# Performance work log

Measured on AMD Instinct MI355X. Metric: run time of the kernel, lower is better.

Reference implementation:

```python
import jax, jax.numpy as jnp
import numpy as np

D = 128       # in_features
H = 256       # hidden
OUT = 128     # out_features
NUM_STEPS = 3
K = 8         # k_neighbors (k = min(K, N))


def setup_inputs() -> dict:
    key = jax.random.key(0)
    ks = jax.random.split(key, 12)
    s = 0.02
    return {
        "x":    jax.random.normal(ks[0], (4, 4096, D), dtype=jnp.float32),
        # neighbor_proj: Linear(D -> H)
        "Wn":   jax.random.normal(ks[1], (D, H), dtype=jnp.float32) * s,
        "bn":   jnp.zeros((H,), dtype=jnp.float32),
        # local_rule[0]: Linear(D + H -> H)
        "W1":   jax.random.normal(ks[2], (D + H, H), dtype=jnp.float32) * s,
        "b1":   jnp.zeros((H,), dtype=jnp.float32),
        # local_rule[1]: LayerNorm(H)
        "ln_g": jnp.ones((H,), dtype=jnp.float32),
        "ln_b": jnp.zeros((H,), dtype=jnp.float32),
        # local_rule[3]: Linear(H -> D)
        "W2":   jax.random.normal(ks[3], (H, D), dtype=jnp.float32) * s,
        "b2":   jnp.zeros((D,), dtype=jnp.float32),
        # out_proj: Linear(D -> OUT)
        "Wo":   jax.random.normal(ks[4], (D, OUT), dtype=jnp.float32) * s,
        "bo":   jnp.zeros((OUT,), dtype=jnp.float32),
    }


def _layernorm(h, g, b, eps=1e-5):
    mu = jnp.mean(h, axis=-1, keepdims=True)
    var = jnp.var(h, axis=-1, keepdims=True)
    return (h - mu) * jax.lax.rsqrt(var + eps) * g + b


def reference(x, Wn, bn, W1, b1, ln_g, ln_b, W2, b2, Wo, bo):
    B, N, _ = x.shape
    k = min(K, N)
    batch_ix = jnp.arange(B)[:, None, None]  # (B,1,1)
    state = x
    for _ in range(NUM_STEPS):
        keys = state @ Wn + bn                                     # (B,N,H)
        keys = keys / jnp.maximum(
            jnp.linalg.norm(keys, axis=-1, keepdims=True), 1e-12)  # F.normalize
        sim = jnp.einsum('bnh,bmh->bnm', keys, keys)               # (B,N,N)
        _, idx = jax.lax.top_k(sim, k)                             # (B,N,k)
        gathered = state[batch_ix, idx]                            # (B,N,k,D)
        neighbor_agg = gathered.mean(axis=2) @ Wn + bn             # (B,N,H)
        combined = jnp.concatenate([state, neighbor_agg], axis=-1) # (B,N,D+H)
        h = _layernorm(combined @ W1 + b1, ln_g, ln_b)
        update = jax.nn.silu(h) @ W2 + b2                          # (B,N,D)
        state = state + update
    return state.mean(axis=1) @ Wo + bo                            # (B,OUT)
```

## Files before the change

### kernel.cpp

```cpp
#include <hip/hip_runtime.h>

#define DDIM 128
#define HDIM 256
#define BQ   4
#define NN   4096
#define RTOT (BQ*NN)

typedef short short8 __attribute__((ext_vector_type(8)));
typedef short short4v __attribute__((ext_vector_type(4)));
typedef float f32x16 __attribute__((ext_vector_type(16)));

__device__ inline unsigned short f2bf(float f) {
    unsigned int u = __float_as_uint(f);
    unsigned int r = (u + 0x7fffu + ((u >> 16) & 1u)) >> 16;
    return (unsigned short)r;
}
__device__ inline float bf2f(unsigned short h) {
    return __uint_as_float(((unsigned int)h) << 16);
}

#define MFMA32(a, b, c) __builtin_amdgcn_mfma_f32_32x32x16_bf16(a, b, c, 0, 0, 0)

__global__ void pack_w_kernel(const float* __restrict__ W, int N,
                              unsigned short* __restrict__ ph, unsigned short* __restrict__ pl) {
    int l = threadIdx.x, l31 = l & 31, lh = l >> 5;
    int nt = N >> 5;
    int t = blockIdx.x / nt, c = blockIdx.x % nt;
    short8 hv, lv;
#pragma unroll
    for (int j = 0; j < 8; ++j) {
        float f = W[(size_t)(t * 16 + lh * 8 + j) * N + c * 32 + l31];
        unsigned short h = f2bf(f);
        hv[j] = (short)h;
        lv[j] = (short)f2bf(f - bf2f(h));
    }
    *(short8*)(ph + (size_t)(blockIdx.x * 64 + l) * 8) = hv;
    *(short8*)(pl + (size_t)(blockIdx.x * 64 + l) * 8) = lv;
}

__global__ __launch_bounds__(256, 2)
void sim_topk_kernel(const unsigned short* __restrict__ khi,
                     const unsigned short* __restrict__ klo,
                     int* __restrict__ idxout) {
    __shared__ __align__(16) char smem[4 * 4 * 4096];

    const int id = blockIdx.x;
    const int xcd = id & 7;
    const int b = xcd >> 1;
    const int j = ((id >> 3) << 1) | (xcd & 1);
    const int rowbase = j * 32;
    const unsigned short* khiB = khi + (size_t)b * NN * HDIM;
    const unsigned short* kloB = klo + (size_t)b * NN * HDIM;

    const int tid = threadIdx.x;
    const int lane = tid & 63, w = tid >> 6;
    const int l31 = lane & 31, lh = lane >> 5;

    short8 ah[16], al[16];
    {
        const unsigned short* ph = khiB + (size_t)(rowbase + l31) * HDIM + lh * 8;
        const unsigned short* pl = kloB + (size_t)(rowbase + l31) * HDIM + lh * 8;
#pragma unroll
        for (int T = 0; T < 16; ++T) {
            ah[T] = *(const short8*)(ph + T * 16);
            al[T] = *(const short8*)(pl + T * 16);
        }
    }
#pragma unroll
    for (int T = 0; T < 16; ++T) {
        asm volatile("" : "+v"(ah[T]));
        asm volatile("" : "+v"(al[T]));
    }

    char* mybuf = smem + w * 16384;

    const int sc8 = lane >> 3, sg8 = lane & 7;
    auto stage = [&](int s) {
        const int cs2 = s >> 3, sub = s & 7;
        const int kb2 = sub >> 1;
        const unsigned short* pb = (sub & 1) ? kloB : khiB;
        char* dst = mybuf + (s & 3) * 4096;
        const int c0 = w * 1024 + cs2 * 32;
#pragma unroll
        for (int i = 0; i < 4; ++i) {
            const unsigned short* src =
                pb + (size_t)(c0 + i * 8 + sc8) * HDIM + kb2 * 64 + ((sg8 ^ sc8) * 8);
            __builtin_amdgcn_global_load_lds(
                (const __attribute__((address_space(1))) void*)src,
                (__attribute__((address_space(3))) void*)(dst + i * 1024), 16, 0, 0);
        }
    };

    stage(0);
    stage(1);
    stage(2);

    const int key = l31 & 7;
    const int rbase = l31 * 128;
    const int sl0 = (((0) * 2 + lh) ^ key) * 16;
    const int sl1 = (((1) * 2 + lh) ^ key) * 16;
    const int sl2 = (((2) * 2 + lh) ^ key) * 16;
    const int sl3 = (((3) * 2 + lh) ^ key) * 16;

    float tv[8]; int ti[8];
#pragma unroll
    for (int s = 0; s < 8; ++s) { tv[s] = -1e30f; ti[s] = 0x7fffffff; }

    for (int cs = 0; cs < 32; ++cs) {
        f32x16 acc;
#pragma unroll
        for (int r = 0; r < 16; ++r) acc[r] = 0.f;

#pragma unroll
        for (int sub = 0; sub < 8; ++sub) {
            const int s = cs * 8 + sub;
            if (s < 254)       asm volatile("s_waitcnt vmcnt(8)" ::: "memory");
            else if (s == 254) asm volatile("s_waitcnt vmcnt(4)" ::: "memory");
            else               asm volatile("s_waitcnt vmcnt(0)" ::: "memory");

            const char* bufc = mybuf + (s & 3) * 4096;
            short8 B0 = *(const short8*)(bufc + rbase + sl0);
            short8 B1 = *(const short8*)(bufc + rbase + sl1);
            short8 B2 = *(const short8*)(bufc + rbase + sl2);
            short8 B3 = *(const short8*)(bufc + rbase + sl3);
            asm volatile("s_waitcnt lgkmcnt(4)" ::: "memory");
            if (s + 3 < 256) stage(s + 3);

            const int T0 = (sub >> 1) * 4;
            if ((sub & 1) == 0) {
                acc = MFMA32(B0, ah[T0],     acc);
                acc = MFMA32(B0, al[T0],     acc);
                acc = MFMA32(B1, ah[T0 + 1], acc);
                acc = MFMA32(B1, al[T0 + 1], acc);
                acc = MFMA32(B2, ah[T0 + 2], acc);
                acc = MFMA32(B2, al[T0 + 2], acc);
                acc = MFMA32(B3, ah[T0 + 3], acc);
                acc = MFMA32(B3, al[T0 + 3], acc);
            } else {
                acc = MFMA32(B0, ah[T0],     acc);
                acc = MFMA32(B1, ah[T0 + 1], acc);
                acc = MFMA32(B2, ah[T0 + 2], acc);
                acc = MFMA32(B3, ah[T0 + 3], acc);
            }
        }

        const int cbase = w * 1024 + cs * 32 + 4 * lh;
#pragma unroll
        for (int r = 0; r < 16; ++r) {
            float v = acc[r];
            int col = cbase + (r & 3) + 8 * (r >> 2);
            if (v > tv[7]) {
                tv[7] = v; ti[7] = col;
#pragma unroll
                for (int q = 7; q >= 1; --q) {
                    if (tv[q] > tv[q - 1]) {
                        float a0 = tv[q]; tv[q] = tv[q - 1]; tv[q - 1] = a0;
                        int   c0_ = ti[q]; ti[q] = ti[q - 1]; ti[q - 1] = c0_;
                    }
                }
            }
        }
    }

    __syncthreads();
    float* vbuf = (float*)smem;
    int*   ibuf = (int*)(smem + 32 * 66 * 4);
    const int list = w * 2 + lh;
#pragma unroll
    for (int s = 0; s < 8; ++s) {
        vbuf[l31 * 66 + list * 8 + s] = tv[s];
        ibuf[l31 * 66 + list * 8 + s] = ti[s];
    }
    __syncthreads();
    if (tid < 32) {
        float fv[8]; int fi[8];
#pragma unroll
        for (int s = 0; s < 8; ++s) { fv[s] = -1e30f; fi[s] = 0x7fffffff; }
        for (int e = 0; e < 64; ++e) {
            float v = vbuf[tid * 66 + e];
            int  ix = ibuf[tid * 66 + e];
            bool ins = (v > fv[7]) || (v == fv[7] && ix < fi[7]);
            if (ins) {
                fv[7] = v; fi[7] = ix;
#pragma unroll
                for (int q = 7; q >= 1; --q) {
                    bool sw = (fv[q] > fv[q - 1]) || (fv[q] == fv[q - 1] && fi[q] < fi[q - 1]);
                    if (sw) {
                        float a0 = fv[q]; fv[q] = fv[q - 1]; fv[q - 1] = a0;
                        int   c0_ = fi[q]; fi[q] = fi[q - 1]; fi[q - 1] = c0_;
                    }
                }
            }
        }
        size_t basei = ((size_t)b * NN + rowbase + tid) * 8;
#pragma unroll
        for (int s = 0; s < 8; ++s) idxout[basei + s] = fi[s];
    }
}

__global__ __launch_bounds__(256, 2)
void gemm_keys_mfma(const float* __restrict__ A,
                    const unsigned short* __restrict__ wh, const unsigned short* __restrict__ wl,
                    const float* __restrict__ bias,
                    unsigned short* __restrict__ khi, unsigned short* __restrict__ klo) {
    __shared__ float ssqbuf[2][32][2];
    const int tid = threadIdx.x, lane = tid & 63, w = tid >> 6;
    const int l31 = lane & 31, lh = lane >> 5;
    const int rw = w & 1, cw = w >> 1;
    const int row = blockIdx.x * 64 + rw * 32 + l31;

    short8 ahi[8], alo[8];
    const float* ap = A + (size_t)row * DDIM + lh * 8;
#pragma unroll
    for (int T = 0; T < 8; ++T) {
        float4 f0 = *(const float4*)(ap + T * 16);
        float4 f1 = *(const float4*)(ap + T * 16 + 4);
        float ff[8] = {f0.x, f0.y, f0.z, f0.w, f1.x, f1.y, f1.z, f1.w};
#pragma unroll
        for (int j2 = 0; j2 < 8; ++j2) {
            unsigned short h = f2bf(ff[j2]);
            ahi[T][j2] = (short)h;
            alo[T][j2] = (short)f2bf(ff[j2] - bf2f(h));
        }
    }

    f32x16 acc[4];
#pragma unroll
    for (int ct = 0; ct < 4; ++ct)
#pragma unroll
        for (int r = 0; r < 16; ++r) acc[ct][r] = 0.f;

#pragma unroll
    for (int T = 0; T < 8; ++T) {
#pragma unroll
        for (int ct = 0; ct < 4; ++ct) {
            const size_t pi = (size_t)((T * 8 + cw * 4 + ct) * 64 + lane) * 8;
            short8 bh = *(const short8*)(wh + pi);
            short8 bl = *(const short8*)(wl + pi);
            acc[ct] = MFMA32(bh, ahi[T], acc[ct]);
            acc[ct] = MFMA32(bl, ahi[T], acc[ct]);
            acc[ct] = MFMA32(bh, alo[T], acc[ct]);
        }
    }

    float ss = 0.f;
#pragma unroll
    for (int ct = 0; ct < 4; ++ct)
#pragma unroll
        for (int g = 0; g < 4; ++g) {
            const int c0 = cw * 128 + ct * 32 + g * 8 + lh * 4;
            float4 bz = *(const float4*)(bias + c0);
            float bzf[4] = {bz.x, bz.y, bz.z, bz.w};
#pragma unroll
            for (int j2 = 0; j2 < 4; ++j2) {
                acc[ct][g * 4 + j2] += bzf[j2];
                ss += acc[ct][g * 4 + j2] * acc[ct][g * 4 + j2];
            }
        }
    ss += __shfl_xor(ss, 32);
    if (lh == 0) ssqbuf[rw][l31][cw] = ss;
    __syncthreads();
    float sstot = ssqbuf[rw][l31][0] + ssqbuf[rw][l31][1];
    float scn = 1.0f / fmaxf(sqrtf(sstot), 1e-12f);

#pragma unroll
    for (int ct = 0; ct < 4; ++ct)
#pragma unroll
        for (int g = 0; g < 4; ++g) {
            const int c0 = cw * 128 + ct * 32 + g * 8 + lh * 4;
            short4v hv, lv;
#pragma unroll
            for (int j2 = 0; j2 < 4; ++j2) {
                float vn = acc[ct][g * 4 + j2] * scn;
                unsigned short h = f2bf(vn);
                hv[j2] = (short)h;
                lv[j2] = (short)f2bf(vn - bf2f(h));
            }
            *(short4v*)(khi + (size_t)row * HDIM + c0) = hv;
            *(short4v*)(klo + (size_t)row * HDIM + c0) = lv;
        }
}

__global__ __launch_bounds__(256, 2)
void gemm_agg_mfma(const float* __restrict__ state, const int* __restrict__ idx,
                   const unsigned short* __restrict__ wh, const unsigned short* __restrict__ wl,
                   const float* __restrict__ bias,
                   unsigned short* __restrict__ oh, unsigned short* __restrict__ ol) {
    const int tid = threadIdx.x, lane = tid & 63, w = tid >> 6;
    const int l31 = lane & 31, lh = lane >> 5;
    const int rw = w & 1, cw = w >> 1;
    const int row = blockIdx.x * 64 + rw * 32 + l31;
    const int bb = row >> 12;
    const float* sb = state + (size_t)bb * NN * DDIM;
    const int* mi = idx + (size_t)row * 8;

    int ridx[8];
#pragma unroll
    for (int k = 0; k < 8; ++k) ridx[k] = mi[k];

    short8 ahi[8], alo[8];
#pragma unroll
    for (int T = 0; T < 8; ++T) {
        float fr[8] = {0.f, 0.f, 0.f, 0.f, 0.f, 0.f, 0.f, 0.f};
#pragma unroll
        for (int k = 0; k < 8; ++k) {
            const float* rp = sb + (size_t)ridx[k] * DDIM + T * 16 + lh * 8;
            float4 f0 = *(const float4*)rp;
            float4 f1 = *(const float4*)(rp + 4);
            fr[0] += f0.x; fr[1] += f0.y; fr[2] += f0.z; fr[3] += f0.w;
            fr[4] += f1.x; fr[5] += f1.y; fr[6] += f1.z; fr[7] += f1.w;
        }
#pragma unroll
        for (int j2 = 0; j2 < 8; ++j2) {
            float v = fr[j2] * 0.125f;
            unsigned short h = f2bf(v);
            ahi[T][j2] = (short)h;
            alo[T][j2] = (short)f2bf(v - bf2f(h));
        }
    }

    f32x16 acc[4];
#pragma unroll
    for (int ct = 0; ct < 4; ++ct)
#pragma unroll
        for (int r = 0; r < 16; ++r) acc[ct][r] = 0.f;

#pragma unroll
    for (int T = 0; T < 8; ++T) {
#pragma unroll
        for (int ct = 0; ct < 4; ++ct) {
            const size_t pi = (size_t)((T * 8 + cw * 4 + ct) * 64 + lane) * 8;
            short8 bh = *(const short8*)(wh + pi);
            short8 bl = *(const short8*)(wl + pi);
            acc[ct] = MFMA32(bh, ahi[T], acc[ct]);
            acc[ct] = MFMA32(bl, ahi[T], acc[ct]);
            acc[ct] = MFMA32(bh, alo[T], acc[ct]);
        }
    }

#pragma unroll
    for (int ct = 0; ct < 4; ++ct)
#pragma unroll
        for (int g = 0; g < 4; ++g) {
            const int c0 = cw * 128 + ct * 32 + g * 8 + lh * 4;
            float4 bz = *(const float4*)(bias + c0);
            float bzf[4] = {bz.x, bz.y, bz.z, bz.w};
            short4v hv, lv;
#pragma unroll
            for (int j2 = 0; j2 < 4; ++j2) {
                float vn = acc[ct][g * 4 + j2] + bzf[j2];
                unsigned short h = f2bf(vn);
                hv[j2] = (short)h;
                lv[j2] = (short)f2bf(vn - bf2f(h));
            }
            *(short4v*)(oh + (size_t)row * HDIM + c0) = hv;
            *(short4v*)(ol + (size_t)row * HDIM + c0) = lv;
        }
}

__global__ __launch_bounds__(256, 2)
void gemm_ln_mfma(const float* __restrict__ state,
                  const unsigned short* __restrict__ agh, const unsigned short* __restrict__ agl,
                  const unsigned short* __restrict__ wh, const unsigned short* __restrict__ wl,
                  const float* __restrict__ b1, const float* __restrict__ lng,
                  const float* __restrict__ lnb,
                  unsigned short* __restrict__ gh, unsigned short* __restrict__ gl) {
    __shared__ float s1buf[2][32][2], s2buf[2][32][2];
    const int tid = threadIdx.x, lane = tid & 63, w = tid >> 6;
    const int l31 = lane & 31, lh = lane >> 5;
    const int rw = w & 1, cw = w >> 1;
    const int row = blockIdx.x * 64 + rw * 32 + l31;

    f32x16 acc[4];
#pragma unroll
    for (int ct = 0; ct < 4; ++ct)
#pragma unroll
        for (int r = 0; r < 16; ++r) acc[ct][r] = 0.f;

    short8 ahi[8], alo[8];
    {
        const float* ap = state + (size_t)row * DDIM + lh * 8;
#pragma unroll
        for (int T = 0; T < 8; ++T) {
            float4 f0 = *(const float4*)(ap + T * 16);
            float4 f1 = *(const float4*)(ap + T * 16 + 4);
            float ff[8] = {f0.x, f0.y, f0.z, f0.w, f1.x, f1.y, f1.z, f1.w};
#pragma unroll
            for (int j2 = 0; j2 < 8; ++j2) {
                unsigned short h = f2bf(ff[j2]);
                ahi[T][j2] = (short)h;
                alo[T][j2] = (short)f2bf(ff[j2] - bf2f(h));
            }
        }
#pragma unroll
        for (int T = 0; T < 8; ++T)
#pragma unroll
            for (int ct = 0; ct < 4; ++ct) {
                const size_t pi = (size_t)((T * 8 + cw * 4 + ct) * 64 + lane) * 8;
                short8 bh = *(const short8*)(wh + pi);
                short8 bl = *(const short8*)(wl + pi);
                acc[ct] = MFMA32(bh, ahi[T], acc[ct]);
                acc[ct] = MFMA32(bl, ahi[T], acc[ct]);
                acc[ct] = MFMA32(bh, alo[T], acc[ct]);
            }
    }
#pragma unroll
    for (int kc = 1; kc < 3; ++kc) {
#pragma unroll
        for (int T = 0; T < 8; ++T) {
            ahi[T] = *(const short8*)(agh + (size_t)row * HDIM + (kc - 1) * 128 + T * 16 + lh * 8);
            alo[T] = *(const short8*)(agl + (size_t)row * HDIM + (kc - 1) * 128 + T * 16 + lh * 8);
        }
#pragma unroll
        for (int T = 0; T < 8; ++T)
#pragma unroll
            for (int ct = 0; ct < 4; ++ct) {
                const size_t pi = (size_t)(((kc * 8 + T) * 8 + cw * 4 + ct) * 64 + lane) * 8;
                short8 bh = *(const short8*)(wh + pi);
                short8 bl = *(const short8*)(wl + pi);
                acc[ct] = MFMA32(bh, ahi[T], acc[ct]);
                acc[ct] = MFMA32(bl, ahi[T], acc[ct]);
                acc[ct] = MFMA32(bh, alo[T], acc[ct]);
            }
    }

    float s1 = 0.f, s2 = 0.f;
#pragma unroll
    for (int ct = 0; ct < 4; ++ct)
#pragma unroll
        for (int g = 0; g < 4; ++g) {
            const int c0 = cw * 128 + ct * 32 + g * 8 + lh * 4;
            float4 bz = *(const float4*)(b1 + c0);
            float bzf[4] = {bz.x, bz.y, bz.z, bz.w};
#pragma unroll
            for (int j2 = 0; j2 < 4; ++j2) {
                acc[ct][g * 4 + j2] += bzf[j2];
                s1 += acc[ct][g * 4 + j2];
                s2 += acc[ct][g * 4 + j2] * acc[ct][g * 4 + j2];
            }
        }
    s1 += __shfl_xor(s1, 32);
    s2 += __shfl_xor(s2, 32);
    if (lh == 0) { s1buf[rw][l31][cw] = s1; s2buf[rw][l31][cw] = s2; }
    __syncthreads();
    float s1t = s1buf[rw][l31][0] + s1buf[rw][l31][1];
    float s2t = s2buf[rw][l31][0] + s2buf[rw][l31][1];
    float mu = s1t * (1.0f / HDIM);
    float var = s2t * (1.0f / HDIM) - mu * mu;
    float inv = 1.0f / sqrtf(var + 1e-5f);

#pragma unroll
    for (int ct = 0; ct < 4; ++ct)
#pragma unroll
        for (int g = 0; g < 4; ++g) {
            const int c0 = cw * 128 + ct * 32 + g * 8 + lh * 4;
            float4 gg = *(const float4*)(lng + c0);
            float4 bb = *(const float4*)(lnb + c0);
            float ggf[4] = {gg.x, gg.y, gg.z, gg.w};
            float bbf[4] = {bb.x, bb.y, bb.z, bb.w};
            short4v hv, lv;
#pragma unroll
            for (int j2 = 0; j2 < 4; ++j2) {
                float hval = (acc[ct][g * 4 + j2] - mu) * inv * ggf[j2] + bbf[j2];
                float gval = hval / (1.0f + expf(-hval));
                unsigned short h = f2bf(gval);
                hv[j2] = (short)h;
                lv[j2] = (short)f2bf(gval - bf2f(h));
            }
            *(short4v*)(gh + (size_t)row * HDIM + c0) = hv;
            *(short4v*)(gl + (size_t)row * HDIM + c0) = lv;
        }
}

__global__ __launch_bounds__(256, 2)
void gemm_upd_mfma(const unsigned short* __restrict__ gh, const unsigned short* __restrict__ gl,
                   const unsigned short* __restrict__ wh, const unsigned short* __restrict__ wl,
                   const float* __restrict__ b2, float* __restrict__ state) {
    const int tid = threadIdx.x, lane = tid & 63, w = tid >> 6;
    const int l31 = lane & 31, lh = lane >> 5;
    const int rw = w & 1, cw = w >> 1;
    const int row = blockIdx.x * 64 + rw * 32 + l31;

    f32x16 acc[2];
#pragma unroll
    for (int ct = 0; ct < 2; ++ct)
#pragma unroll
        for (int r = 0; r < 16; ++r) acc[ct][r] = 0.f;

    short8 ahi[8], alo[8];
#pragma unroll
    for (int kc = 0; kc < 2; ++kc) {
#pragma unroll
        for (int T = 0; T < 8; ++T) {
            ahi[T] = *(const short8*)(gh + (size_t)row * HDIM + kc * 128 + T * 16 + lh * 8);
            alo[T] = *(const short8*)(gl + (size_t)row * HDIM + kc * 128 + T * 16 + lh * 8);
        }
#pragma unroll
        for (int T = 0; T < 8; ++T)
#pragma unroll
            for (int ct = 0; ct < 2; ++ct) {
                const size_t pi = (size_t)(((kc * 8 + T) * 4 + cw * 2 + ct) * 64 + lane) * 8;
                short8 bh = *(const short8*)(wh + pi);
                short8 bl = *(const short8*)(wl + pi);
                acc[ct] = MFMA32(bh, ahi[T], acc[ct]);
                acc[ct] = MFMA32(bl, ahi[T], acc[ct]);
                acc[ct] = MFMA32(bh, alo[T], acc[ct]);
            }
    }

#pragma unroll
    for (int ct = 0; ct < 2; ++ct)
#pragma unroll
        for (int g = 0; g < 4; ++g) {
            const int c0 = cw * 64 + ct * 32 + g * 8 + lh * 4;
            float4 bz = *(const float4*)(b2 + c0);
            float bzf[4] = {bz.x, bz.y, bz.z, bz.w};
            float4* sp = (float4*)(state + (size_t)row * DDIM + c0);
            float4 sv = *sp;
            float svf[4] = {sv.x, sv.y, sv.z, sv.w};
#pragma unroll
            for (int j2 = 0; j2 < 4; ++j2) svf[j2] += acc[ct][g * 4 + j2] + bzf[j2];
            sv.x = svf[0]; sv.y = svf[1]; sv.z = svf[2]; sv.w = svf[3];
            *sp = sv;
        }
}

__global__ void partial_mean_kernel(const float* __restrict__ state, float* __restrict__ partial) {
    int b = blockIdx.y, seg = blockIdx.x, tid = threadIdx.x;
    const float* sp = state + ((size_t)b * NN + (size_t)seg * 128) * DDIM;
    float acc = 0.f;
    for (int i = 0; i < 128; ++i) acc += sp[(size_t)i * DDIM + tid];
    partial[((size_t)b * 32 + seg) * DDIM + tid] = acc;
}

__global__ void final_out_kernel(const float* __restrict__ partial, const float* __restrict__ Wo,
                                 const float* __restrict__ bo, float* __restrict__ out) {
    __shared__ float mean[BQ][DDIM];
    int tid = threadIdx.x;
    for (int o = tid; o < BQ * DDIM; o += 256) {
        int b = o >> 7, d = o & 127;
        float s = 0.f;
        for (int p = 0; p < 32; ++p) s += partial[((size_t)b * 32 + p) * DDIM + d];
        mean[b][d] = s * (1.0f / NN);
    }
    __syncthreads();
    for (int o = tid; o < BQ * DDIM; o += 256) {
        int b = o >> 7, c = o & 127;
        float acc = bo[c];
        for (int d = 0; d < DDIM; ++d) acc += mean[b][d] * Wo[d * DDIM + c];
        out[o] = acc;
    }
}

extern "C" void kernel_launch(void* const* d_in, const int* in_sizes, int n_in,
                              void* d_out, int out_size, void* d_ws, size_t ws_size,
                              hipStream_t stream) {
    const float* x   = (const float*)d_in[0];
    const float* Wn  = (const float*)d_in[1];
    const float* bn  = (const float*)d_in[2];
    const float* W1  = (const float*)d_in[3];
    const float* b1  = (const float*)d_in[4];
    const float* lng = (const float*)d_in[5];
    const float* lnb = (const float*)d_in[6];
    const float* W2  = (const float*)d_in[7];
    const float* b2  = (const float*)d_in[8];
    const float* Wo  = (const float*)d_in[9];
    const float* bo  = (const float*)d_in[10];
    float* out = (float*)d_out;

    float* ws    = (float*)d_ws;
    float* state = ws;
    unsigned short* agghi = (unsigned short*)(state + (size_t)RTOT * DDIM);
    unsigned short* agglo = agghi + (size_t)RTOT * HDIM;
    unsigned short* khi_b = agglo + (size_t)RTOT * HDIM;
    unsigned short* klo_b = khi_b + (size_t)RTOT * HDIM;
    unsigned short* ghi = khi_b;
    unsigned short* glo = klo_b;
    float* partial = (float*)(klo_b + (size_t)RTOT * HDIM);
    int*   idxbuf  = (int*)(partial + (size_t)BQ * 32 * DDIM);
    unsigned short* wnh = (unsigned short*)(idxbuf + (size_t)RTOT * 8);
    unsigned short* wnl = wnh + 128 * 256;
    unsigned short* w1h = wnl + 128 * 256;
    unsigned short* w1l = w1h + 384 * 256;
    unsigned short* w2h = w1l + 384 * 256;
    unsigned short* w2l = w2h + 256 * 128;

    hipMemcpyAsync(state, x, (size_t)RTOT * DDIM * sizeof(float),
                   hipMemcpyDeviceToDevice, stream);

    pack_w_kernel<<<(128 / 16) * (256 / 32), 64, 0, stream>>>(Wn, 256, wnh, wnl);
    pack_w_kernel<<<(384 / 16) * (256 / 32), 64, 0, stream>>>(W1, 256, w1h, w1l);
    pack_w_kernel<<<(256 / 16) * (128 / 32), 64, 0, stream>>>(W2, 128, w2h, w2l);

    for (int step = 0; step < 3; ++step) {
        gemm_keys_mfma<<<RTOT / 64, 256, 0, stream>>>(state, wnh, wnl, bn, khi_b, klo_b);
        sim_topk_kernel<<<512, 256, 0, stream>>>(khi_b, klo_b, idxbuf);
        gemm_agg_mfma<<<RTOT / 64, 256, 0, stream>>>(state, idxbuf, wnh, wnl, bn, agghi, agglo);
        gemm_ln_mfma<<<RTOT / 64, 256, 0, stream>>>(state, agghi, agglo, w1h, w1l,
                                                    b1, lng, lnb, ghi, glo);
        gemm_upd_mfma<<<RTOT / 64, 256, 0, stream>>>(ghi, glo, w2h, w2l, b2, state);
    }
    partial_mean_kernel<<<dim3(32, BQ), 128, 0, stream>>>(state, partial);
    final_out_kernel<<<1, 256, 0, stream>>>(partial, Wo, bo, out);
}
```

Baseline: 863.3 us.

## Tile sim_topk as 64 rows by half columns with shared LDS staging and split merge

```diff
diff --git a/kernel.cpp b/kernel.cpp
--- a/kernel.cpp
+++ b/kernel.cpp
@@ -38,28 +38,32 @@
     *(short8*)(pl + (size_t)(blockIdx.x * 64 + l) * 8) = lv;
 }
 
-__global__ __launch_bounds__(256, 2)
+__global__ __launch_bounds__(512, 4)
 void sim_topk_kernel(const unsigned short* __restrict__ khi,
                      const unsigned short* __restrict__ klo,
-                     int* __restrict__ idxout) {
+                     float* __restrict__ svals, int* __restrict__ sidx) {
     __shared__ __align__(16) char smem[4 * 4 * 4096];
 
     const int id = blockIdx.x;
     const int xcd = id & 7;
     const int b = xcd >> 1;
     const int j = ((id >> 3) << 1) | (xcd & 1);
-    const int rowbase = j * 32;
+    const int rowgroup = j >> 1;
+    const int ch = j & 1;
+    const int rowbase = rowgroup * 64;
+    const int colbase = ch * 2048;
     const unsigned short* khiB = khi + (size_t)b * NN * HDIM;
     const unsigned short* kloB = klo + (size_t)b * NN * HDIM;
 
     const int tid = threadIdx.x;
     const int lane = tid & 63, w = tid >> 6;
     const int l31 = lane & 31, lh = lane >> 5;
+    const int rw = w & 1, cw = w >> 1;
 
     short8 ah[16], al[16];
     {
-        const unsigned short* ph = khiB + (size_t)(rowbase + l31) * HDIM + lh * 8;
-        const unsigned short* pl = kloB + (size_t)(rowbase + l31) * HDIM + lh * 8;
+        const unsigned short* ph = khiB + (size_t)(rowbase + rw * 32 + l31) * HDIM + lh * 8;
+        const unsigned short* pl = kloB + (size_t)(rowbase + rw * 32 + l31) * HDIM + lh * 8;
 #pragma unroll
         for (int T = 0; T < 16; ++T) {
             ah[T] = *(const short8*)(ph + T * 16);
@@ -72,17 +76,18 @@
         asm volatile("" : "+v"(al[T]));
     }
 
-    char* mybuf = smem + w * 16384;
+    char* gbuf = smem + cw * 16384;
 
     const int sc8 = lane >> 3, sg8 = lane & 7;
     auto stage = [&](int s) {
         const int cs2 = s >> 3, sub = s & 7;
         const int kb2 = sub >> 1;
         const unsigned short* pb = (sub & 1) ? kloB : khiB;
-        char* dst = mybuf + (s & 3) * 4096;
-        const int c0 = w * 1024 + cs2 * 32;
-#pragma unroll
-        for (int i = 0; i < 4; ++i) {
+        char* dst = gbuf + (s & 3) * 4096;
+        const int c0 = colbase + cw * 512 + cs2 * 32;
+#pragma unroll
+        for (int ii = 0; ii < 2; ++ii) {
+            const int i = rw * 2 + ii;
             const unsigned short* src =
                 pb + (size_t)(c0 + i * 8 + sc8) * HDIM + kb2 * 64 + ((sg8 ^ sc8) * 8);
             __builtin_amdgcn_global_load_lds(
@@ -97,16 +102,16 @@
 
     const int key = l31 & 7;
     const int rbase = l31 * 128;
-    const int sl0 = (((0) * 2 + lh) ^ key) * 16;
-    const int sl1 = (((1) * 2 + lh) ^ key) * 16;
-    const int sl2 = (((2) * 2 + lh) ^ key) * 16;
-    const int sl3 = (((3) * 2 + lh) ^ key) * 16;
+    const int sl0 = ((0 * 2 + lh) ^ key) * 16;
+    const int sl1 = ((1 * 2 + lh) ^ key) * 16;
+    const int sl2 = ((2 * 2 + lh) ^ key) * 16;
+    const int sl3 = ((3 * 2 + lh) ^ key) * 16;
 
     float tv[8]; int ti[8];
 #pragma unroll
     for (int s = 0; s < 8; ++s) { tv[s] = -1e30f; ti[s] = 0x7fffffff; }
 
-    for (int cs = 0; cs < 32; ++cs) {
+    for (int cs = 0; cs < 16; ++cs) {
         f32x16 acc;
 #pragma unroll
         for (int r = 0; r < 16; ++r) acc[r] = 0.f;
@@ -114,17 +119,18 @@
 #pragma unroll
         for (int sub = 0; sub < 8; ++sub) {
             const int s = cs * 8 + sub;
-            if (s < 254)       asm volatile("s_waitcnt vmcnt(8)" ::: "memory");
-            else if (s == 254) asm volatile("s_waitcnt vmcnt(4)" ::: "memory");
+            if (s < 126)       asm volatile("s_waitcnt vmcnt(4)" ::: "memory");
+            else if (s == 126) asm volatile("s_waitcnt vmcnt(2)" ::: "memory");
             else               asm volatile("s_waitcnt vmcnt(0)" ::: "memory");
-
-            const char* bufc = mybuf + (s & 3) * 4096;
+            __builtin_amdgcn_s_barrier();
+            __builtin_amdgcn_sched_barrier(0);
+
+            const char* bufc = gbuf + (s & 3) * 4096;
             short8 B0 = *(const short8*)(bufc + rbase + sl0);
             short8 B1 = *(const short8*)(bufc + rbase + sl1);
             short8 B2 = *(const short8*)(bufc + rbase + sl2);
             short8 B3 = *(const short8*)(bufc + rbase + sl3);
-            asm volatile("s_waitcnt lgkmcnt(4)" ::: "memory");
-            if (s + 3 < 256) stage(s + 3);
+            if (s + 3 < 128) stage(s + 3);
 
             const int T0 = (sub >> 1) * 4;
             if ((sub & 1) == 0) {
@@ -144,7 +150,7 @@
             }
         }
 
-        const int cbase = w * 1024 + cs * 32 + 4 * lh;
+        const int cbase = colbase + cw * 512 + cs * 32 + 4 * lh;
 #pragma unroll
         for (int r = 0; r < 16; ++r) {
             float v = acc[r];
@@ -164,15 +170,16 @@
 
     __syncthreads();
     float* vbuf = (float*)smem;
-    int*   ibuf = (int*)(smem + 32 * 66 * 4);
-    const int list = w * 2 + lh;
+    int*   ibuf = (int*)(smem + 64 * 66 * 4);
+    const int list = cw * 2 + lh;
+    const int mrow = rw * 32 + l31;
 #pragma unroll
     for (int s = 0; s < 8; ++s) {
-        vbuf[l31 * 66 + list * 8 + s] = tv[s];
-        ibuf[l31 * 66 + list * 8 + s] = ti[s];
+        vbuf[mrow * 66 + list * 8 + s] = tv[s];
+        ibuf[mrow * 66 + list * 8 + s] = ti[s];
     }
     __syncthreads();
-    if (tid < 32) {
+    if (tid < 64) {
         float fv[8]; int fi[8];
 #pragma unroll
         for (int s = 0; s < 8; ++s) { fv[s] = -1e30f; fi[s] = 0x7fffffff; }
@@ -192,9 +199,9 @@
                 }
             }
         }
-        size_t basei = ((size_t)b * NN + rowbase + tid) * 8;
-#pragma unroll
-        for (int s = 0; s < 8; ++s) idxout[basei + s] = fi[s];
+        const size_t lb = ((size_t)(b * NN + rowbase + tid) * 2 + ch) * 8;
+#pragma unroll
+        for (int s = 0; s < 8; ++s) { svals[lb + s] = fv[s]; sidx[lb + s] = fi[s]; }
     }
 }
 
@@ -282,21 +289,48 @@
 }
 
 __global__ __launch_bounds__(256, 2)
-void gemm_agg_mfma(const float* __restrict__ state, const int* __restrict__ idx,
+void gemm_agg_mfma(const float* __restrict__ state,
+                   const float* __restrict__ svals, const int* __restrict__ sidx,
                    const unsigned short* __restrict__ wh, const unsigned short* __restrict__ wl,
                    const float* __restrict__ bias,
                    unsigned short* __restrict__ oh, unsigned short* __restrict__ ol) {
+    __shared__ int mslot[256][8];
     const int tid = threadIdx.x, lane = tid & 63, w = tid >> 6;
     const int l31 = lane & 31, lh = lane >> 5;
     const int rw = w & 1, cw = w >> 1;
     const int row = blockIdx.x * 64 + rw * 32 + l31;
     const int bb = row >> 12;
     const float* sb = state + (size_t)bb * NN * DDIM;
-    const int* mi = idx + (size_t)row * 8;
 
     int ridx[8];
-#pragma unroll
-    for (int k = 0; k < 8; ++k) ridx[k] = mi[k];
+    {
+        const size_t lb = (size_t)row * 16;
+        float av[8], bv[8]; int ai[8], bi2[8];
+#pragma unroll
+        for (int k = 0; k < 8; ++k) {
+            av[k] = svals[lb + k];     ai[k]  = sidx[lb + k];
+            bv[k] = svals[lb + 8 + k]; bi2[k] = sidx[lb + 8 + k];
+        }
+        int* ms = mslot[tid];
+#pragma unroll
+        for (int i2 = 0; i2 < 8; ++i2) {
+            int r = i2;
+#pragma unroll
+            for (int j2 = 0; j2 < 8; ++j2)
+                r += ((bv[j2] > av[i2]) || (bv[j2] == av[i2] && bi2[j2] < ai[i2])) ? 1 : 0;
+            if (r < 8) ms[r] = ai[i2];
+        }
+#pragma unroll
+        for (int j2 = 0; j2 < 8; ++j2) {
+            int r = j2;
+#pragma unroll
+            for (int i2 = 0; i2 < 8; ++i2)
+                r += ((av[i2] > bv[j2]) || (av[i2] == bv[j2] && ai[i2] < bi2[j2])) ? 1 : 0;
+            if (r < 8) ms[r] = bi2[j2];
+        }
+#pragma unroll
+        for (int k = 0; k < 8; ++k) ridx[k] = ms[k];
+    }
 
     short8 ahi[8], alo[8];
 #pragma unroll
@@ -577,8 +611,9 @@
     unsigned short* ghi = khi_b;
     unsigned short* glo = klo_b;
     float* partial = (float*)(klo_b + (size_t)RTOT * HDIM);
-    int*   idxbuf  = (int*)(partial + (size_t)BQ * 32 * DDIM);
-    unsigned short* wnh = (unsigned short*)(idxbuf + (size_t)RTOT * 8);
+    float* svals   = partial + (size_t)BQ * 32 * DDIM;
+    int*   sidx    = (int*)(svals + (size_t)RTOT * 16);
+    unsigned short* wnh = (unsigned short*)(sidx + (size_t)RTOT * 16);
     unsigned short* wnl = wnh + 128 * 256;
     unsigned short* w1h = wnl + 128 * 256;
     unsigned short* w1l = w1h + 384 * 256;
@@ -594,8 +629,9 @@
 
     for (int step = 0; step < 3; ++step) {
         gemm_keys_mfma<<<RTOT / 64, 256, 0, stream>>>(state, wnh, wnl, bn, khi_b, klo_b);
-        sim_topk_kernel<<<512, 256, 0, stream>>>(khi_b, klo_b, idxbuf);
-        gemm_agg_mfma<<<RTOT / 64, 256, 0, stream>>>(state, idxbuf, wnh, wnl, bn, agghi, agglo);
+        sim_topk_kernel<<<512, 512, 0, stream>>>(khi_b, klo_b, svals, sidx);
+        gemm_agg_mfma<<<RTOT / 64, 256, 0, stream>>>(state, svals, sidx, wnh, wnl, bn,
+                                                     agghi, agglo);
         gemm_ln_mfma<<<RTOT / 64, 256, 0, stream>>>(state, agghi, agglo, w1h, w1l,
                                                     b1, lng, lnb, ghi, glo);
         gemm_upd_mfma<<<RTOT / 64, 256, 0, stream>>>(ghi, glo, w2h, w2l, b2, state);
```

Result: slower. 1.321 ms (+53.1%).
